# Performance work log

Hardware: AMD Instinct MI355X
Metric: run time of the kernel (lower is better)

The kernel has to match this reference:

```python
import jax, jax.numpy as jnp
import numpy as np

N_NODES = 100000

def gcn_conv(x, edge_index, W, b):
    # GCNConv with normalize=True and self-loops:
    # out = D^{-1/2} (A + I) D^{-1/2} (x W) + b
    h = x @ W                                   # [N, out]
    src, dst = edge_index[0], edge_index[1]
    deg = jax.ops.segment_sum(jnp.ones(src.shape[0], h.dtype), dst,
                              num_segments=N_NODES) + 1.0  # +1 for self loop
    dinv = jax.lax.rsqrt(deg)
    norm = dinv[src] * dinv[dst]                # [E]
    agg = jax.ops.segment_sum(h[src] * norm[:, None], dst,
                              num_segments=N_NODES)        # [N, out]
    agg = agg + h * (1.0 / deg)[:, None]        # self-loop term: norm_ii = 1/deg_i
    return agg + b


def setup_inputs() -> dict:
    key = jax.random.key(0)
    k0, k1, k2, k3 = jax.random.split(key, 4)
    N, E, F_IN, H, C = N_NODES, 1600000, 256, 128, 40
    x = jax.random.normal(k0, (N, F_IN), dtype=jnp.float32)
    edge_index = jax.random.randint(k1, (2, E), 0, N, dtype=jnp.int64)
    W1 = jax.random.normal(k2, (F_IN, H), dtype=jnp.float32) * (1.0 / np.sqrt(F_IN))
    b1 = jnp.zeros((H,), jnp.float32)
    W2 = jax.random.normal(k3, (H, C), dtype=jnp.float32) * (1.0 / np.sqrt(H))
    b2 = jnp.zeros((C,), jnp.float32)
    return {"x": x, "edge_index": edge_index, "W1": W1, "b1": b1, "W2": W2, "b2": b2}


def reference(x, edge_index, W1, b1, W2, b2):
    # layer 1 + ReLU (dropout = identity in eval mode)
    h = jax.nn.relu(gcn_conv(x, edge_index, W1, b1))
    # final layer (no activation)
    return gcn_conv(h, edge_index, W2, b2)
```

## Files before the change

### kernel.cpp

```cpp
#include <hip/hip_runtime.h>
#include <hip/hip_bf16.h>


#define FIN 256
#define HDIM 128
#define CDIM 40
#define CAP 8192
#define EC 8192

typedef __attribute__((ext_vector_type(8))) short bf16x8;
typedef __attribute__((ext_vector_type(4))) float f32x4;

__device__ inline short f2bf(float f) {
    unsigned u = __float_as_uint(f);
    unsigned r = (u + 0x7FFFu + ((u >> 16) & 1u)) >> 16;
    return (short)r;
}
__device__ inline float bflo(unsigned u) { return __uint_as_float(u << 16); }
__device__ inline float bfhi(unsigned u) { return __uint_as_float(u & 0xFFFF0000u); }

__global__ __launch_bounds__(1024) void p1_hist_k(const int* __restrict__ ei, int* __restrict__ mat,
                                                  int E, int NBUCK) {
    __shared__ int hist[512];
    for (int t = threadIdx.x; t < NBUCK; t += 1024) hist[t] = 0;
    __syncthreads();
    int e0 = blockIdx.x * EC;
#pragma unroll
    for (int k = 0; k < EC; k += 1024) {
        int e = e0 + k + threadIdx.x;
        if (e < E) atomicAdd(&hist[ei[E + e] >> 8], 1);
    }
    __syncthreads();
    for (int t = threadIdx.x; t < NBUCK; t += 1024) mat[blockIdx.x * NBUCK + t] = hist[t];
}

__global__ __launch_bounds__(64) void scan_cols_k(int* __restrict__ mat, int* __restrict__ bcnt,
                                                  int NB1, int NBUCK) {
    int b = blockIdx.x;
    int lane = threadIdx.x;
    int carry = b * CAP;
    for (int c0 = 0; c0 < NB1; c0 += 64) {
        int idx = c0 + lane;
        int v = (idx < NB1) ? mat[idx * NBUCK + b] : 0;
        int incl = v;
#pragma unroll
        for (int off = 1; off < 64; off <<= 1) {
            int t = __shfl_up(incl, off);
            if (lane >= off) incl += t;
        }
        if (idx < NB1) mat[idx * NBUCK + b] = carry + (incl - v);
        carry += __shfl(incl, 63);
    }
    if (lane == 0) bcnt[b] = carry - b * CAP;
}

__global__ __launch_bounds__(1024) void p1_scatter_k(const int* __restrict__ ei, const int* __restrict__ mat,
                                                     int* __restrict__ bmem, int E, int NBUCK) {
    __shared__ int base[512];
    for (int t = threadIdx.x; t < NBUCK; t += 1024) base[t] = mat[blockIdx.x * NBUCK + t];
    __syncthreads();
    int e0 = blockIdx.x * EC;
#pragma unroll
    for (int k = 0; k < EC; k += 1024) {
        int e = e0 + k + threadIdx.x;
        if (e < E) {
            int s = ei[e];
            int d = ei[E + e];
            int pos = atomicAdd(&base[d >> 8], 1);
            bmem[pos] = s | ((d & 255) << 20);
        }
    }
}

__global__ __launch_bounds__(256) void p2_build_k(const int* __restrict__ bmem, const int* __restrict__ bcnt,
                                                  int* __restrict__ csr, int2* __restrict__ nseg,
                                                  float* __restrict__ dinv, float* __restrict__ invd, int N) {
    __shared__ int hist[256], cur[256], sc[256];
    __shared__ int stage[CAP];
    const int b = blockIdx.x;
    const int tid = threadIdx.x;
    int cnt = bcnt[b];
    if (cnt > CAP) cnt = CAP;
    const int* src = bmem + b * CAP;
    hist[tid] = 0;
    __syncthreads();
    for (int j = tid; j < cnt; j += 256) atomicAdd(&hist[src[j] >> 20], 1);
    __syncthreads();
    int v = hist[tid];
    sc[tid] = v;
    __syncthreads();
    for (int off = 1; off < 256; off <<= 1) {
        int t = (tid >= off) ? sc[tid - off] : 0;
        __syncthreads();
        sc[tid] += t;
        __syncthreads();
    }
    int excl = sc[tid] - v;
    cur[tid] = excl;
    int i = b * 256 + tid;
    if (i < N) {
        nseg[i] = make_int2(b * CAP + excl, v);
        float dg = (float)(v + 1);
        dinv[i] = rsqrtf(dg);
        invd[i] = 1.0f / dg;
    }
    __syncthreads();
    for (int j = tid; j < cnt; j += 256) {
        int rec = src[j];
        int pos = atomicAdd(&cur[rec >> 20], 1);
        stage[pos] = rec & 0xFFFFF;
    }
    __syncthreads();
    int* dst = csr + b * CAP;
    for (int j = tid; j < cnt; j += 256) dst[j] = stage[j];
}

__global__ __launch_bounds__(256) void castW_k(const float* __restrict__ W1, const float* __restrict__ W2,
                                               short* __restrict__ W1T, short* __restrict__ W2T) {
    int idx = blockIdx.x * 256 + threadIdx.x;
    if (idx < FIN * HDIM) {
        int k = idx >> 7, n = idx & 127;
        W1T[n * FIN + k] = f2bf(W1[idx]);
    } else {
        int j = idx - FIN * HDIM;
        if (j < 48 * HDIM) {
            int c = j >> 7, k = j & 127;
            W2T[j] = (c < CDIM) ? f2bf(W2[k * CDIM + c]) : (short)0;
        }
    }
}

#define LDSTRIDE 40
__global__ __launch_bounds__(256) void gemm1_mfma_k(const float* __restrict__ X,
                                                    const short* __restrict__ W1T,
                                                    short* __restrict__ T1b, int N) {
    __shared__ short As[128 * LDSTRIDE];
    __shared__ short Bs[128 * LDSTRIDE];
    const int tid = threadIdx.x;
    const int lane = tid & 63;
    const int wid = tid >> 6;
    const int w0 = wid & 1, w1 = wid >> 1;
    const int quad = lane >> 4;
    const int l16 = lane & 15;
    const int rowbase = blockIdx.x * 128;
    const int sr = tid >> 1;
    const int sh = tid & 1;

    f32x4 acc[4][4];
#pragma unroll
    for (int a = 0; a < 4; a++)
#pragma unroll
        for (int b = 0; b < 4; b++) acc[a][b] = (f32x4){0.f, 0.f, 0.f, 0.f};

    const int arow = min(rowbase + sr, N - 1);
    const float* xsrc = X + (size_t)arow * FIN + sh * 16;
    const int4* bsrc = (const int4*)(W1T + (size_t)sr * FIN + sh * 16);

    for (int k0 = 0; k0 < FIN; k0 += 32) {
        float vals[16];
        *(float4*)&vals[0]  = *(const float4*)(xsrc + k0);
        *(float4*)&vals[4]  = *(const float4*)(xsrc + k0 + 4);
        *(float4*)&vals[8]  = *(const float4*)(xsrc + k0 + 8);
        *(float4*)&vals[12] = *(const float4*)(xsrc + k0 + 12);
        short tmp[16];
#pragma unroll
        for (int c = 0; c < 16; c++) tmp[c] = f2bf(vals[c]);
        ((int4*)&As[sr * LDSTRIDE + sh * 16])[0] = ((int4*)tmp)[0];
        ((int4*)&As[sr * LDSTRIDE + sh * 16])[1] = ((int4*)tmp)[1];
        int4 b0 = bsrc[k0 >> 3];
        int4 b1 = bsrc[(k0 >> 3) + 1];
        ((int4*)&Bs[sr * LDSTRIDE + sh * 16])[0] = b0;
        ((int4*)&Bs[sr * LDSTRIDE + sh * 16])[1] = b1;
        __syncthreads();

        bf16x8 afr[4], bfr[4];
#pragma unroll
        for (int mt = 0; mt < 4; mt++)
            afr[mt] = *(const bf16x8*)&As[(w1 * 64 + mt * 16 + l16) * LDSTRIDE + quad * 8];
#pragma unroll
        for (int nt = 0; nt < 4; nt++)
            bfr[nt] = *(const bf16x8*)&Bs[(w0 * 64 + nt * 16 + l16) * LDSTRIDE + quad * 8];
#pragma unroll
        for (int mt = 0; mt < 4; mt++)
#pragma unroll
            for (int nt = 0; nt < 4; nt++)
                acc[mt][nt] = __builtin_amdgcn_mfma_f32_16x16x32_bf16(afr[mt], bfr[nt], acc[mt][nt], 0, 0, 0);
        __syncthreads();
    }
#pragma unroll
    for (int mt = 0; mt < 4; mt++) {
#pragma unroll
        for (int r = 0; r < 4; r++) {
            int row = rowbase + w1 * 64 + mt * 16 + quad * 4 + r;
            if (row < N) {
#pragma unroll
                for (int nt = 0; nt < 4; nt++) {
                    int col = w0 * 64 + nt * 16 + l16;
                    T1b[(size_t)row * HDIM + col] = f2bf(acc[mt][nt][r]);
                }
            }
        }
    }
}

__global__ __launch_bounds__(256) void agg1_k(const short* __restrict__ T1b, const int2* __restrict__ nseg,
                                              const int* __restrict__ csr, const float* __restrict__ dinv,
                                              const float* __restrict__ invd, const float* __restrict__ b1,
                                              unsigned* __restrict__ Hb, int N) {
    const int lane = threadIdx.x & 63;
    const int quad = lane >> 4;
    const int ql = lane & 15;
    const int i = blockIdx.x * 4 + (threadIdx.x >> 6);
    if (i >= N) return;
    const int2 sg = nseg[i];
    const int e0 = sg.x, deg = sg.y;
    int sv = 0; float wv = 0.f;
    if (lane < deg) { sv = csr[e0 + lane]; wv = dinv[sv]; }

    const uint4* rowp = (const uint4*)T1b;
    float acc[8];
#pragma unroll
    for (int t = 0; t < 8; t++) acc[t] = 0.f;

    const int dmain = deg < 64 ? deg : 64;
    for (int j = 0; j < dmain; j += 4) {
        int idx = j + quad;
        int sj = __shfl(sv, idx);
        float wj = __shfl(wv, idx);
        wj = (idx < dmain) ? wj : 0.f;
        uint4 u = rowp[sj * 16 + ql];
        acc[0] += wj * bflo(u.x); acc[1] += wj * bfhi(u.x);
        acc[2] += wj * bflo(u.y); acc[3] += wj * bfhi(u.y);
        acc[4] += wj * bflo(u.z); acc[5] += wj * bfhi(u.z);
        acc[6] += wj * bflo(u.w); acc[7] += wj * bfhi(u.w);
    }
    const int eEnd = e0 + deg;
    for (int e = e0 + 64; e < eEnd; e += 4) {
        int idx = e + quad;
        int cl = idx < eEnd ? idx : eEnd - 1;
        int sj = csr[cl];
        float wj = (idx < eEnd) ? dinv[sj] : 0.f;
        uint4 u = rowp[sj * 16 + ql];
        acc[0] += wj * bflo(u.x); acc[1] += wj * bfhi(u.x);
        acc[2] += wj * bflo(u.y); acc[3] += wj * bfhi(u.y);
        acc[4] += wj * bflo(u.z); acc[5] += wj * bfhi(u.z);
        acc[6] += wj * bflo(u.w); acc[7] += wj * bfhi(u.w);
    }
#pragma unroll
    for (int t = 0; t < 8; t++) {
        acc[t] += __shfl_xor(acc[t], 16);
        acc[t] += __shfl_xor(acc[t], 32);
    }
    const float di = dinv[i], sf = invd[i];
    uint4 us = rowp[i * 16 + ql];
    float4 bA = *(const float4*)(b1 + ql * 8);
    float4 bB = *(const float4*)(b1 + ql * 8 + 4);
    float o0 = fmaxf(bA.x + sf * bflo(us.x) + di * acc[0], 0.f);
    float o1 = fmaxf(bA.y + sf * bfhi(us.x) + di * acc[1], 0.f);
    float o2 = fmaxf(bA.z + sf * bflo(us.y) + di * acc[2], 0.f);
    float o3 = fmaxf(bA.w + sf * bfhi(us.y) + di * acc[3], 0.f);
    float o4 = fmaxf(bB.x + sf * bflo(us.z) + di * acc[4], 0.f);
    float o5 = fmaxf(bB.y + sf * bfhi(us.z) + di * acc[5], 0.f);
    float o6 = fmaxf(bB.z + sf * bflo(us.w) + di * acc[6], 0.f);
    float o7 = fmaxf(bB.w + sf * bfhi(us.w) + di * acc[7], 0.f);
    uint4 pk;
    pk.x = ((unsigned)(unsigned short)f2bf(o0)) | (((unsigned)(unsigned short)f2bf(o1)) << 16);
    pk.y = ((unsigned)(unsigned short)f2bf(o2)) | (((unsigned)(unsigned short)f2bf(o3)) << 16);
    pk.z = ((unsigned)(unsigned short)f2bf(o4)) | (((unsigned)(unsigned short)f2bf(o5)) << 16);
    pk.w = ((unsigned)(unsigned short)f2bf(o6)) | (((unsigned)(unsigned short)f2bf(o7)) << 16);
    if (quad == 0) ((uint4*)(Hb + (size_t)i * 64))[ql] = pk;
}

__global__ __launch_bounds__(256) void gemm2_mfma_k(const short* __restrict__ Hb,
                                                    const short* __restrict__ W2T,
                                                    float* __restrict__ T2, int N) {
    __shared__ short As[128 * LDSTRIDE];
    __shared__ short Bs[48 * LDSTRIDE];
    const int tid = threadIdx.x;
    const int lane = tid & 63;
    const int wid = tid >> 6;
    const int quad = lane >> 4;
    const int l16 = lane & 15;
    const int rowbase = blockIdx.x * 128;
    const int sr = tid >> 1;
    const int sh = tid & 1;

    f32x4 acc[2][3];
#pragma unroll
    for (int a = 0; a < 2; a++)
#pragma unroll
        for (int b = 0; b < 3; b++) acc[a][b] = (f32x4){0.f, 0.f, 0.f, 0.f};

    const int arow = min(rowbase + sr, N - 1);
    const int4* asrc = (const int4*)(Hb + (size_t)arow * HDIM + sh * 16);
    const int br = tid >> 1, bh = tid & 1;
    const int4* bsrc = (const int4*)(W2T + br * HDIM + bh * 16);

    for (int k0 = 0; k0 < HDIM; k0 += 32) {
        int4 a0 = asrc[k0 >> 3];
        int4 a1 = asrc[(k0 >> 3) + 1];
        ((int4*)&As[sr * LDSTRIDE + sh * 16])[0] = a0;
        ((int4*)&As[sr * LDSTRIDE + sh * 16])[1] = a1;
        if (tid < 96) {
            int4 b0 = bsrc[k0 >> 3];
            int4 b1 = bsrc[(k0 >> 3) + 1];
            ((int4*)&Bs[br * LDSTRIDE + bh * 16])[0] = b0;
            ((int4*)&Bs[br * LDSTRIDE + bh * 16])[1] = b1;
        }
        __syncthreads();
        bf16x8 afr[2], bfr[3];
#pragma unroll
        for (int mt = 0; mt < 2; mt++)
            afr[mt] = *(const bf16x8*)&As[(wid * 32 + mt * 16 + l16) * LDSTRIDE + quad * 8];
#pragma unroll
        for (int nt = 0; nt < 3; nt++)
            bfr[nt] = *(const bf16x8*)&Bs[(nt * 16 + l16) * LDSTRIDE + quad * 8];
#pragma unroll
        for (int mt = 0; mt < 2; mt++)
#pragma unroll
            for (int nt = 0; nt < 3; nt++)
                acc[mt][nt] = __builtin_amdgcn_mfma_f32_16x16x32_bf16(afr[mt], bfr[nt], acc[mt][nt], 0, 0, 0);
        __syncthreads();
    }
#pragma unroll
    for (int mt = 0; mt < 2; mt++) {
#pragma unroll
        for (int r = 0; r < 4; r++) {
            int row = rowbase + wid * 32 + mt * 16 + quad * 4 + r;
            if (row < N) {
#pragma unroll
                for (int nt = 0; nt < 3; nt++) {
                    int col = nt * 16 + l16;
                    if (col < CDIM) T2[(size_t)row * CDIM + col] = acc[mt][nt][r];
                }
            }
        }
    }
}

__global__ __launch_bounds__(256) void agg2_k(const float* __restrict__ T2, const int2* __restrict__ nseg,
                                              const int* __restrict__ csr, const float* __restrict__ dinv,
                                              const float* __restrict__ invd, const float* __restrict__ b2,
                                              float* __restrict__ OUT, int N) {
    const int lane = threadIdx.x & 63;
    const int quad = lane >> 4;
    const int qlr = lane & 15;
    const int ql = qlr < 10 ? qlr : 9;
    const bool act = qlr < 10;
    const int i = blockIdx.x * 4 + (threadIdx.x >> 6);
    if (i >= N) return;
    const int2 sg = nseg[i];
    const int e0 = sg.x, deg = sg.y;
    int sv = 0; float wv = 0.f;
    if (lane < deg) { sv = csr[e0 + lane]; wv = dinv[sv]; }
    float acc[4] = {0.f, 0.f, 0.f, 0.f};
    const int dmain = deg < 64 ? deg : 64;
    for (int j = 0; j < dmain; j += 4) {
        int idx = j + quad;
        int sj = __shfl(sv, idx);
        float wj = __shfl(wv, idx);
        wj = (idx < dmain && act) ? wj : 0.f;
        float4 v = *(const float4*)(T2 + sj * CDIM + ql * 4);
        acc[0] += wj * v.x; acc[1] += wj * v.y; acc[2] += wj * v.z; acc[3] += wj * v.w;
    }
    const int eEnd = e0 + deg;
    for (int e = e0 + 64; e < eEnd; e += 4) {
        int idx = e + quad;
        int cl = idx < eEnd ? idx : eEnd - 1;
        int sj = csr[cl];
        float wj = (idx < eEnd && act) ? dinv[sj] : 0.f;
        float4 v = *(const float4*)(T2 + sj * CDIM + ql * 4);
        acc[0] += wj * v.x; acc[1] += wj * v.y; acc[2] += wj * v.z; acc[3] += wj * v.w;
    }
#pragma unroll
    for (int t = 0; t < 4; t++) {
        acc[t] += __shfl_xor(acc[t], 16);
        acc[t] += __shfl_xor(acc[t], 32);
    }
    const float di = dinv[i], sf = invd[i];
    float4 vs = *(const float4*)(T2 + (size_t)i * CDIM + ql * 4);
    float4 bb = *(const float4*)(b2 + ql * 4);
    float4 o;
    o.x = bb.x + sf * vs.x + di * acc[0];
    o.y = bb.y + sf * vs.y + di * acc[1];
    o.z = bb.z + sf * vs.z + di * acc[2];
    o.w = bb.w + sf * vs.w + di * acc[3];
    if (quad == 0 && act) *(float4*)(OUT + (size_t)i * CDIM + qlr * 4) = o;
}

extern "C" void kernel_launch(void* const* d_in, const int* in_sizes, int n_in,
                              void* d_out, int out_size, void* d_ws, size_t ws_size,
                              hipStream_t stream) {
    const float* x   = (const float*)d_in[0];
    const int*   ei  = (const int*)d_in[1];
    const float* W1  = (const float*)d_in[2];
    const float* b1  = (const float*)d_in[3];
    const float* W2  = (const float*)d_in[4];
    const float* b2  = (const float*)d_in[5];
    float*       out = (float*)d_out;

    const int Hd  = in_sizes[3];
    const int Fin = in_sizes[2] / Hd;
    const int N   = in_sizes[0] / Fin;
    const int E   = in_sizes[1] / 2;

    const int NBUCK = (N + 255) / 256;
    const int NB1   = (E + EC - 1) / EC;

    char* base = (char*)d_ws;
    size_t off = 0;
    auto alloc = [&](size_t bytes) -> void* {
        void* p = base + off;
        off += (bytes + 255) & ~(size_t)255;
        return p;
    };
    size_t matB  = (size_t)NB1 * NBUCK * 4;
    size_t bmemB = (size_t)NBUCK * CAP * 4;
    size_t t1bB  = (size_t)N * HDIM * 2;
    size_t regA  = matB + 256 + bmemB;
    if (t1bB > regA) regA = t1bB;
    char* pA = (char*)alloc(regA);
    int*   mat  = (int*)pA;
    int*   bmem = (int*)(pA + ((matB + 255) & ~(size_t)255));
    short* t1b  = (short*)pA;

    int*      bcnt = (int*)alloc((size_t)NBUCK * 4);
    int*      csr  = (int*)alloc((size_t)NBUCK * CAP * 4);
    int2*     nseg = (int2*)alloc((size_t)N * 8);
    float*    dinv = (float*)alloc((size_t)N * 4);
    float*    invd = (float*)alloc((size_t)N * 4);
    short*    W1T  = (short*)alloc((size_t)HDIM * FIN * 2);
    short*    W2T  = (short*)alloc((size_t)48 * HDIM * 2);
    unsigned* hb   = (unsigned*)alloc((size_t)N * HDIM * 2);
    float*    t2   = (float*)alloc((size_t)N * CDIM * 4);

    p1_hist_k<<<NB1, 1024, 0, stream>>>(ei, mat, E, NBUCK);
    scan_cols_k<<<NBUCK, 64, 0, stream>>>(mat, bcnt, NB1, NBUCK);
    p1_scatter_k<<<NB1, 1024, 0, stream>>>(ei, mat, bmem, E, NBUCK);
    p2_build_k<<<NBUCK, 256, 0, stream>>>(bmem, bcnt, csr, nseg, dinv, invd, N);
    castW_k<<<(FIN * HDIM + 48 * HDIM + 255) / 256, 256, 0, stream>>>(W1, W2, W1T, W2T);

    gemm1_mfma_k<<<(N + 127) / 128, 256, 0, stream>>>(x, W1T, t1b, N);
    agg1_k<<<(N + 3) / 4, 256, 0, stream>>>(t1b, nseg, csr, dinv, invd, b1, hb, N);
    gemm2_mfma_k<<<(N + 127) / 128, 256, 0, stream>>>((const short*)hb, W2T, t2, N);
    agg2_k<<<(N + 3) / 4, 256, 0, stream>>>(t2, nseg, csr, dinv, invd, b2, out, N);
}
```

Baseline: 360.6 us.

## Store layer-2 transform as padded bf16 and unroll agg1 gather loop

gemm2 now writes its output as bf16 rows padded to 48 columns instead of fp32 rows of 40, which cuts the bytes agg2 gathers per neighbor roughly in half. agg2 is reorganised so that 8-lane groups each read one 96-byte row as 16-byte chunks, with a two-neighbor unroll and an extra reduction step. agg1's main neighbor loop is unrolled four times so more independent row loads are in flight at once. The cost is bf16 rounding of the pre-aggregation layer-2 features, which adds precision error, plus higher register pressure from the unrolling.

```diff
diff --git a/kernel.cpp b/kernel.cpp
--- a/kernel.cpp
+++ b/kernel.cpp
@@ -223,16 +223,28 @@
     for (int t = 0; t < 8; t++) acc[t] = 0.f;
 
     const int dmain = deg < 64 ? deg : 64;
-    for (int j = 0; j < dmain; j += 4) {
-        int idx = j + quad;
-        int sj = __shfl(sv, idx);
-        float wj = __shfl(wv, idx);
-        wj = (idx < dmain) ? wj : 0.f;
-        uint4 u = rowp[sj * 16 + ql];
-        acc[0] += wj * bflo(u.x); acc[1] += wj * bfhi(u.x);
-        acc[2] += wj * bflo(u.y); acc[3] += wj * bfhi(u.y);
-        acc[4] += wj * bflo(u.z); acc[5] += wj * bfhi(u.z);
-        acc[6] += wj * bflo(u.w); acc[7] += wj * bfhi(u.w);
+    for (int j = 0; j < dmain; j += 16) {
+        const int i0 = j + quad, i1 = j + 4 + quad, i2 = j + 8 + quad, i3 = j + 12 + quad;
+        int s0 = __shfl(sv, i0); int s1 = __shfl(sv, i1);
+        int s2 = __shfl(sv, i2); int s3 = __shfl(sv, i3);
+        float w0 = __shfl(wv, i0); float w1 = __shfl(wv, i1);
+        float w2 = __shfl(wv, i2); float w3 = __shfl(wv, i3);
+        w0 = (i0 < dmain) ? w0 : 0.f;
+        w1 = (i1 < dmain) ? w1 : 0.f;
+        w2 = (i2 < dmain) ? w2 : 0.f;
+        w3 = (i3 < dmain) ? w3 : 0.f;
+        uint4 u0 = rowp[s0 * 16 + ql];
+        uint4 u1 = rowp[s1 * 16 + ql];
+        uint4 u2 = rowp[s2 * 16 + ql];
+        uint4 u3 = rowp[s3 * 16 + ql];
+        acc[0] += w0 * bflo(u0.x) + w1 * bflo(u1.x) + w2 * bflo(u2.x) + w3 * bflo(u3.x);
+        acc[1] += w0 * bfhi(u0.x) + w1 * bfhi(u1.x) + w2 * bfhi(u2.x) + w3 * bfhi(u3.x);
+        acc[2] += w0 * bflo(u0.y) + w1 * bflo(u1.y) + w2 * bflo(u2.y) + w3 * bflo(u3.y);
+        acc[3] += w0 * bfhi(u0.y) + w1 * bfhi(u1.y) + w2 * bfhi(u2.y) + w3 * bfhi(u3.y);
+        acc[4] += w0 * bflo(u0.z) + w1 * bflo(u1.z) + w2 * bflo(u2.z) + w3 * bflo(u3.z);
+        acc[5] += w0 * bfhi(u0.z) + w1 * bfhi(u1.z) + w2 * bfhi(u2.z) + w3 * bfhi(u3.z);
+        acc[6] += w0 * bflo(u0.w) + w1 * bflo(u1.w) + w2 * bflo(u2.w) + w3 * bflo(u3.w);
+        acc[7] += w0 * bfhi(u0.w) + w1 * bfhi(u1.w) + w2 * bfhi(u2.w) + w3 * bfhi(u3.w);
     }
     const int eEnd = e0 + deg;
     for (int e = e0 + 64; e < eEnd; e += 4) {
@@ -273,7 +285,7 @@
 
 __global__ __launch_bounds__(256) void gemm2_mfma_k(const short* __restrict__ Hb,
                                                     const short* __restrict__ W2T,
-                                                    float* __restrict__ T2, int N) {
+                                                    short* __restrict__ T2b, int N) {
     __shared__ short As[128 * LDSTRIDE];
     __shared__ short Bs[48 * LDSTRIDE];
     const int tid = threadIdx.x;
@@ -331,61 +343,87 @@
 #pragma unroll
                 for (int nt = 0; nt < 3; nt++) {
                     int col = nt * 16 + l16;
-                    if (col < CDIM) T2[(size_t)row * CDIM + col] = acc[mt][nt][r];
+                    T2b[(size_t)row * 48 + col] = f2bf(acc[mt][nt][r]);
                 }
             }
         }
     }
 }
 
-__global__ __launch_bounds__(256) void agg2_k(const float* __restrict__ T2, const int2* __restrict__ nseg,
+__global__ __launch_bounds__(256) void agg2_k(const short* __restrict__ T2b, const int2* __restrict__ nseg,
                                               const int* __restrict__ csr, const float* __restrict__ dinv,
                                               const float* __restrict__ invd, const float* __restrict__ b2,
                                               float* __restrict__ OUT, int N) {
     const int lane = threadIdx.x & 63;
-    const int quad = lane >> 4;
-    const int qlr = lane & 15;
-    const int ql = qlr < 10 ? qlr : 9;
-    const bool act = qlr < 10;
+    const int oct = lane >> 3;
+    const int olr = lane & 7;
+    const int ol = olr < 6 ? olr : 5;
+    const bool act = olr < 6;
     const int i = blockIdx.x * 4 + (threadIdx.x >> 6);
     if (i >= N) return;
     const int2 sg = nseg[i];
     const int e0 = sg.x, deg = sg.y;
     int sv = 0; float wv = 0.f;
     if (lane < deg) { sv = csr[e0 + lane]; wv = dinv[sv]; }
-    float acc[4] = {0.f, 0.f, 0.f, 0.f};
+
+    const uint4* rowp = (const uint4*)T2b;
+    float acc[8];
+#pragma unroll
+    for (int t = 0; t < 8; t++) acc[t] = 0.f;
+
     const int dmain = deg < 64 ? deg : 64;
-    for (int j = 0; j < dmain; j += 4) {
-        int idx = j + quad;
-        int sj = __shfl(sv, idx);
-        float wj = __shfl(wv, idx);
-        wj = (idx < dmain && act) ? wj : 0.f;
-        float4 v = *(const float4*)(T2 + sj * CDIM + ql * 4);
-        acc[0] += wj * v.x; acc[1] += wj * v.y; acc[2] += wj * v.z; acc[3] += wj * v.w;
+    for (int j = 0; j < dmain; j += 16) {
+        const int i0 = j + oct, i1 = j + 8 + oct;
+        int s0 = __shfl(sv, i0); int s1 = __shfl(sv, i1);
+        float w0 = __shfl(wv, i0); float w1 = __shfl(wv, i1);
+        w0 = (i0 < dmain && act) ? w0 : 0.f;
+        w1 = (i1 < dmain && act) ? w1 : 0.f;
+        uint4 u0 = rowp[s0 * 6 + ol];
+        uint4 u1 = rowp[s1 * 6 + ol];
+        acc[0] += w0 * bflo(u0.x) + w1 * bflo(u1.x);
+        acc[1] += w0 * bfhi(u0.x) + w1 * bfhi(u1.x);
+        acc[2] += w0 * bflo(u0.y) + w1 * bflo(u1.y);
+        acc[3] += w0 * bfhi(u0.y) + w1 * bfhi(u1.y);
+        acc[4] += w0 * bflo(u0.z) + w1 * bflo(u1.z);
+        acc[5] += w0 * bfhi(u0.z) + w1 * bfhi(u1.z);
+        acc[6] += w0 * bflo(u0.w) + w1 * bflo(u1.w);
+        acc[7] += w0 * bfhi(u0.w) + w1 * bfhi(u1.w);
     }
     const int eEnd = e0 + deg;
-    for (int e = e0 + 64; e < eEnd; e += 4) {
-        int idx = e + quad;
+    for (int e = e0 + 64; e < eEnd; e += 8) {
+        int idx = e + oct;
         int cl = idx < eEnd ? idx : eEnd - 1;
         int sj = csr[cl];
         float wj = (idx < eEnd && act) ? dinv[sj] : 0.f;
-        float4 v = *(const float4*)(T2 + sj * CDIM + ql * 4);
-        acc[0] += wj * v.x; acc[1] += wj * v.y; acc[2] += wj * v.z; acc[3] += wj * v.w;
-    }
-#pragma unroll
-    for (int t = 0; t < 4; t++) {
+        uint4 u = rowp[sj * 6 + ol];
+        acc[0] += wj * bflo(u.x); acc[1] += wj * bfhi(u.x);
+        acc[2] += wj * bflo(u.y); acc[3] += wj * bfhi(u.y);
+        acc[4] += wj * bflo(u.z); acc[5] += wj * bfhi(u.z);
+        acc[6] += wj * bflo(u.w); acc[7] += wj * bfhi(u.w);
+    }
+#pragma unroll
+    for (int t = 0; t < 8; t++) {
+        acc[t] += __shfl_xor(acc[t], 8);
         acc[t] += __shfl_xor(acc[t], 16);
         acc[t] += __shfl_xor(acc[t], 32);
     }
-    const float di = dinv[i], sf = invd[i];
-    float4 vs = *(const float4*)(T2 + (size_t)i * CDIM + ql * 4);
-    float4 bb = *(const float4*)(b2 + ql * 4);
-    float4 o;
-    o.x = bb.x + sf * vs.x + di * acc[0];
-    o.y = bb.y + sf * vs.y + di * acc[1];
-    o.z = bb.z + sf * vs.z + di * acc[2];
-    o.w = bb.w + sf * vs.w + di * acc[3];
-    if (quad == 0 && act) *(float4*)(OUT + (size_t)i * CDIM + qlr * 4) = o;
+    if (oct == 0 && olr < 5) {
+        const float di = dinv[i], sf = invd[i];
+        uint4 us = rowp[i * 6 + olr];
+        float4 bA = *(const float4*)(b2 + olr * 8);
+        float4 bB = *(const float4*)(b2 + olr * 8 + 4);
+        float4 oA, oB;
+        oA.x = bA.x + sf * bflo(us.x) + di * acc[0];
+        oA.y = bA.y + sf * bfhi(us.x) + di * acc[1];
+        oA.z = bA.z + sf * bflo(us.y) + di * acc[2];
+        oA.w = bA.w + sf * bfhi(us.y) + di * acc[3];
+        oB.x = bB.x + sf * bflo(us.z) + di * acc[4];
+        oB.y = bB.y + sf * bfhi(us.z) + di * acc[5];
+        oB.z = bB.z + sf * bflo(us.w) + di * acc[6];
+        oB.w = bB.w + sf * bfhi(us.w) + di * acc[7];
+        *(float4*)(OUT + (size_t)i * CDIM + olr * 8) = oA;
+        *(float4*)(OUT + (size_t)i * CDIM + olr * 8 + 4) = oB;
+    }
 }
 
 extern "C" void kernel_launch(void* const* d_in, const int* in_sizes, int n_in,
@@ -432,7 +470,7 @@
     short*    W1T  = (short*)alloc((size_t)HDIM * FIN * 2);
     short*    W2T  = (short*)alloc((size_t)48 * HDIM * 2);
     unsigned* hb   = (unsigned*)alloc((size_t)N * HDIM * 2);
-    float*    t2   = (float*)alloc((size_t)N * CDIM * 4);
+    short*    t2b  = (short*)alloc((size_t)N * 48 * 2);
 
     p1_hist_k<<<NB1, 1024, 0, stream>>>(ei, mat, E, NBUCK);
     scan_cols_k<<<NBUCK, 64, 0, stream>>>(mat, bcnt, NB1, NBUCK);
@@ -442,6 +480,6 @@
 
     gemm1_mfma_k<<<(N + 127) / 128, 256, 0, stream>>>(x, W1T, t1b, N);
     agg1_k<<<(N + 3) / 4, 256, 0, stream>>>(t1b, nseg, csr, dinv, invd, b1, hb, N);
-    gemm2_mfma_k<<<(N + 127) / 128, 256, 0, stream>>>((const short*)hb, W2T, t2, N);
-    agg2_k<<<(N + 3) / 4, 256, 0, stream>>>(t2, nseg, csr, dinv, invd, b2, out, N);
-}
+    gemm2_mfma_k<<<(N + 127) / 128, 256, 0, stream>>>((const short*)hb, W2T, t2b, N);
+    agg2_k<<<(N + 3) / 4, 256, 0, stream>>>(t2b, nseg, csr, dinv, invd, b2, out, N);
+}
```

After: 338.7 us. 1.06x faster.
